# Kernel optimization log

Measured on AMD Instinct MI355X. Metric: run time of the kernel, lower is better.

Reference implementation:

```python
import jax, jax.numpy as jnp
import numpy as np

H = 4
HD = 32
C = 128
NU = 40000
NI = 40000
E = 200000


def _linear(x, W, b):
    # torch Linear: y = x @ W.T + b, W is [out, in]
    return x @ W.T + b


def _counts_in(query, sorted_keys):
    l = jnp.searchsorted(sorted_keys, query, side='left')
    r = jnp.searchsorted(sorted_keys, query, side='right')
    return (r - l).astype(jnp.float32)


def _segment_softmax(scores, seg, n):
    # scores: [E, H], seg: [E] destination ids
    m = jax.ops.segment_max(scores, seg, num_segments=n)
    m = jnp.where(jnp.isfinite(m), m, 0.0)
    e = jnp.exp(scores - m[seg])
    z = jax.ops.segment_sum(e, seg, num_segments=n)
    return e / z[seg]


def _deg_count(idx, n):
    return jnp.zeros((n,), jnp.float32).at[idx].add(1.0)


def _layernorm(x):
    mu = x.mean(-1, keepdims=True)
    var = ((x - mu) ** 2).mean(-1, keepdims=True)
    return (x - mu) / jnp.sqrt(var + 1e-5)


def _relation(x_src, x_dst, src, dst, t_src, t_dst,
              Wq, bq, Wk, bk, Wv, bv, Wo, bo,
              head_bias, beta, tau_raw, gamma, delta,
              counts, recips, n_dst):
    Q = _linear(x_dst, Wq, bq).reshape(-1, H, HD)
    K = _linear(x_src, Wk, bk).reshape(-1, H, HD)
    V = _linear(x_src, Wv, bv).reshape(-1, H, HD)
    Qe, Ke, Ve = Q[dst], K[src], V[src]                      # [E, H, HD]
    scores = (Qe * Ke).sum(-1) / jnp.sqrt(jnp.float32(HD))   # [E, H]
    scores = scores + head_bias
    dt = jnp.abs(t_dst[dst] - t_src[src]) + 1e-6
    tau = jax.nn.softplus(tau_raw) + 1e-6
    scores = scores + (-jnp.log1p(dt / tau))[:, None] * beta
    scores = scores + jnp.log1p(counts)[:, None] * gamma
    scores = scores + recips[:, None] * delta
    w = _segment_softmax(scores, dst, n_dst)                 # [E, H]
    out_e = (Ve * w[:, :, None]).reshape(-1, C)
    out_e = _linear(out_e, Wo, bo)
    return jnp.zeros((n_dst, C), x_dst.dtype).at[dst].add(out_e)


def setup_inputs() -> dict:
    key = jax.random.key(0)
    ks = jax.random.split(key, 20)
    inp = {
        'x_user': jax.random.normal(ks[0], (NU, C), jnp.float32),
        'x_item': jax.random.normal(ks[1], (NI, C), jnp.float32),
        't_user': jax.random.uniform(ks[2], (NU,), jnp.float32) * 100.0,
        't_item': jax.random.uniform(ks[3], (NI,), jnp.float32) * 100.0,
        'edge_index_ui': jax.random.randint(ks[4], (2, E), 0, NU, jnp.int32),
        'edge_index_iu': jax.random.randint(ks[5], (2, E), 0, NI, jnp.int32),
        'Wq': jax.random.normal(ks[6], (C, C), jnp.float32) * 0.05,
        'bq': jax.random.normal(ks[7], (C,), jnp.float32) * 0.05,
        'Wk': jax.random.normal(ks[8], (C, C), jnp.float32) * 0.05,
        'bk': jax.random.normal(ks[9], (C,), jnp.float32) * 0.05,
        'Wv': jax.random.normal(ks[10], (C, C), jnp.float32) * 0.05,
        'bv': jax.random.normal(ks[11], (C,), jnp.float32) * 0.05,
        'Wo': jax.random.normal(ks[12], (C, C), jnp.float32) * 0.05,
        'bo': jax.random.normal(ks[13], (C,), jnp.float32) * 0.05,
        'rel_head_bias': jax.random.normal(ks[14], (2, H), jnp.float32) * 0.1,
        'time_beta': jax.random.normal(ks[15], (2, H), jnp.float32) * 0.1,
        'time_tau_raw': jax.random.normal(ks[16], (2,), jnp.float32),
        'gamma_multirel': jax.random.normal(ks[17], (2, H), jnp.float32) * 0.1,
        'delta_recip': jax.random.normal(ks[18], (2, H), jnp.float32) * 0.1,
    }
    return inp


def reference(x_user, x_item, t_user, t_item, edge_index_ui, edge_index_iu,
              Wq, bq, Wk, bk, Wv, bv, Wo, bo,
              rel_head_bias, time_beta, time_tau_raw, gamma_multirel, delta_recip):
    su, du = edge_index_ui[0], edge_index_ui[1]   # user -> item
    si, di = edge_index_iu[0], edge_index_iu[1]   # item -> user
    # multirel counts (pair multiplicity - 1) and reciprocity flags, per relation
    pid_ui = su * NI + du            # (user,item) pair ids (fits int32: NU*NI < 2^31)
    pid_iu = si * NU + di            # (item,user) pair ids
    rev_for_ui = di * NI + si        # reversed pairs of iu edges in (user,item) space
    rev_for_iu = du * NU + su        # reversed pairs of ui edges in (item,user) space
    counts_ui = _counts_in(pid_ui, jnp.sort(pid_ui)) - 1.0
    counts_iu = _counts_in(pid_iu, jnp.sort(pid_iu)) - 1.0
    recips_ui = (_counts_in(pid_ui, jnp.sort(rev_for_ui)) > 0).astype(jnp.float32)
    recips_iu = (_counts_in(pid_iu, jnp.sort(rev_for_iu)) > 0).astype(jnp.float32)

    out_item = _relation(x_user, x_item, su, du, t_user, t_item,
                         Wq, bq, Wk, bk, Wv, bv, Wo, bo,
                         rel_head_bias[0], time_beta[0], time_tau_raw[0],
                         gamma_multirel[0], delta_recip[0], counts_ui, recips_ui, NI)
    out_user = _relation(x_item, x_user, si, di, t_item, t_user,
                         Wq, bq, Wk, bk, Wv, bv, Wo, bo,
                         rel_head_bias[1], time_beta[1], time_tau_raw[1],
                         gamma_multirel[1], delta_recip[1], counts_iu, recips_iu, NU)
    # degree centrality bias: total (in + out) degree added to every channel
    deg_user = _deg_count(su, NU) + _deg_count(di, NU)
    deg_item = _deg_count(du, NI) + _deg_count(si, NI)
    out_user = out_user + deg_user[:, None]
    out_item = out_item + deg_item[:, None]
    return _layernorm(out_user + x_user), _layernorm(out_item + x_item)
```

## Files before the change

### kernel.cpp

```cpp
#include <hip/hip_runtime.h>
#include <math.h>

constexpr int kH  = 4;
constexpr int kHD = 32;
constexpr int kC  = 128;
constexpr int kNU = 40000;
constexpr int kNI = 40000;
constexpr int kE  = 200000;
constexpr int kNT = kNU + kNI;
constexpr int kSB = (kNT + 1023) / 1024;
constexpr int kTilesPerSide = kNU / 16;
constexpr int kTiles = kNT / 16;
constexpr int kGemmBlocks  = 768;
constexpr int kTableBlocks = 1536;
constexpr int kFusedBlocks = 2304;

#define DEV_INLINE __device__ __forceinline__

typedef short bf16x8 __attribute__((ext_vector_type(8)));
typedef float f32x4  __attribute__((ext_vector_type(4)));
typedef uint32_t u32x4 __attribute__((ext_vector_type(4)));
typedef unsigned long long u64;

DEV_INLINE unsigned short f2bf(float f) {
  uint32_t u = __float_as_uint(f);
  u += 0x7fffu + ((u >> 16) & 1u);
  return (unsigned short)(u >> 16);
}

DEV_INLINE float bflo(uint32_t u) { return __uint_as_float(u << 16); }
DEV_INLINE float bfhi(uint32_t u) { return __uint_as_float(u & 0xffff0000u); }

DEV_INLINE int swz(int row, int elem) {
  return (elem & 7) | (((elem >> 3) ^ (row & 7)) << 3);
}

DEV_INLINE int rpf(const int* __restrict__ rp, const int* __restrict__ boff, int i) {
  return rp[i] + boff[i >> 10];
}

__global__ void cast4w_bf16(const float* __restrict__ w0, const float* __restrict__ w1,
                            const float* __restrict__ w2, const float* __restrict__ w3,
                            unsigned short* __restrict__ o0, unsigned short* __restrict__ o1,
                            unsigned short* __restrict__ o2, unsigned short* __restrict__ o3) {
  int i = blockIdx.x * blockDim.x + threadIdx.x;
  int m = i >> 12, j = i & 4095;
  const float* in = (m == 0) ? w0 : (m == 1) ? w1 : (m == 2) ? w2 : w3;
  unsigned short* out = (m == 0) ? o0 : (m == 1) ? o1 : (m == 2) ? o2 : o3;
  float4 v = ((const float4*)in)[j];
  ushort4 o = {f2bf(v.x), f2bf(v.y), f2bf(v.z), f2bf(v.w)};
  ((ushort4*)out)[j] = o;
}

__global__ __launch_bounds__(256, 3) void qkv_build(
    const float* __restrict__ Xu, const float* __restrict__ Xi,
    const unsigned short* __restrict__ Wq, const unsigned short* __restrict__ Wk,
    const unsigned short* __restrict__ Wv,
    const float* __restrict__ bq, const float* __restrict__ bk,
    const float* __restrict__ bv,
    unsigned short* __restrict__ Qu, unsigned short* __restrict__ Ku,
    unsigned short* __restrict__ Vu,
    unsigned short* __restrict__ Qi, unsigned short* __restrict__ Ki,
    unsigned short* __restrict__ Vi,
    const int* __restrict__ du, const int* __restrict__ di,
    int* __restrict__ deg_all, int* __restrict__ pos_all) {
  __shared__ unsigned short sx[16 * kC];
  __shared__ unsigned short sr[3 * 16 * kC];
  const int bid = blockIdx.x;
  const int tid = threadIdx.x;

  if (bid % 3 != 1) {
    const int tb = (bid / 3) * 2 + ((bid % 3) ? 1 : 0);
    for (int t = tb * 256 + tid; t < 2 * kE; t += kTableBlocks * 256) {
      if (t < kE) {
        pos_all[t] = atomicAdd(&deg_all[du[t]], 1);
      } else {
        pos_all[t] = atomicAdd(&deg_all[kNI + di[t - kE]], 1);
      }
    }
    return;
  }

  const int gb   = bid / 3;
  const int wave = tid >> 6;
  const int lane = tid & 63;
  const int mr   = lane & 15;
  const int quad = lane >> 4;
  const int ct0  = wave * 2;
  const int srow = tid >> 4;
  const int schk = tid & 15;

  bf16x8 wf[3][2][4];
  {
    const unsigned short* Ws[3] = {Wq, Wk, Wv};
#pragma unroll
    for (int m = 0; m < 3; ++m)
#pragma unroll
      for (int c = 0; c < 2; ++c) {
        const unsigned short* wrow = Ws[m] + (size_t)((ct0 + c) * 16 + mr) * kC + quad * 8;
#pragma unroll
        for (int kc = 0; kc < 4; ++kc) wf[m][c][kc] = *(const bf16x8*)(wrow + kc * 32);
      }
  }

  int tile = gb;
  float4 xa, xb;
  {
    const bool item = tile >= kTilesPerSide;
    const float* X = item ? Xi : Xu;
    const int base = (item ? tile - kTilesPerSide : tile) * 16;
    const float* xr = X + (size_t)(base + srow) * kC + schk * 8;
    xa = ((const float4*)xr)[0];
    xb = ((const float4*)xr)[1];
  }

  for (; tile < kTiles; tile += kGemmBlocks) {
    const bool item = tile >= kTilesPerSide;
    const int base = (item ? tile - kTilesPerSide : tile) * 16;

    {
      bf16x8 p;
      p[0] = (short)f2bf(xa.x); p[1] = (short)f2bf(xa.y);
      p[2] = (short)f2bf(xa.z); p[3] = (short)f2bf(xa.w);
      p[4] = (short)f2bf(xb.x); p[5] = (short)f2bf(xb.y);
      p[6] = (short)f2bf(xb.z); p[7] = (short)f2bf(xb.w);
      *(bf16x8*)(sx + srow * kC + ((schk ^ (srow & 7)) << 3)) = p;
    }
    __syncthreads();

    bf16x8 b[4];
#pragma unroll
    for (int kc = 0; kc < 4; ++kc)
      b[kc] = *(const bf16x8*)(sx + mr * kC + (((quad + kc * 4) ^ (mr & 7)) << 3));

    int ntile = tile + kGemmBlocks;
    if (ntile < kTiles) {
      const bool nit = ntile >= kTilesPerSide;
      const float* X = nit ? Xi : Xu;
      const int nbase = (nit ? ntile - kTilesPerSide : ntile) * 16;
      const float* xr = X + (size_t)(nbase + srow) * kC + schk * 8;
      xa = ((const float4*)xr)[0];
      xb = ((const float4*)xr)[1];
    }

    f32x4 acc[3][2];
#pragma unroll
    for (int m = 0; m < 3; ++m) {
      acc[m][0] = (f32x4){0.f, 0.f, 0.f, 0.f};
      acc[m][1] = (f32x4){0.f, 0.f, 0.f, 0.f};
    }
#pragma unroll
    for (int kc = 0; kc < 4; ++kc)
#pragma unroll
      for (int m = 0; m < 3; ++m)
#pragma unroll
        for (int c = 0; c < 2; ++c)
          acc[m][c] = __builtin_amdgcn_mfma_f32_16x16x32_bf16(wf[m][c][kc], b[kc], acc[m][c], 0, 0, 0);

    const float* bs[3] = {bq, bk, bv};
#pragma unroll
    for (int m = 0; m < 3; ++m)
#pragma unroll
      for (int c = 0; c < 2; ++c) {
        int c0 = (ct0 + c) * 16 + quad * 4;
        float4 bb = *(const float4*)(bs[m] + c0);
        uint2 p;
        p.x = (uint32_t)f2bf(acc[m][c][0] + bb.x) | ((uint32_t)f2bf(acc[m][c][1] + bb.y) << 16);
        p.y = (uint32_t)f2bf(acc[m][c][2] + bb.z) | ((uint32_t)f2bf(acc[m][c][3] + bb.w) << 16);
        *(uint2*)(sr + (m * 16 + mr) * kC + swz(mr, c0)) = p;
      }
    __syncthreads();

    {
      unsigned short* Os[3] = {item ? Qi : Qu, item ? Ki : Ku, item ? Vi : Vu};
      const int el = (schk ^ (srow & 7)) << 3;
#pragma unroll
      for (int m = 0; m < 3; ++m) {
        bf16x8 v = *(const bf16x8*)(sr + (m * 16 + srow) * kC + el);
        *(bf16x8*)(Os[m] + (size_t)(base + srow) * kC + schk * 8) = v;
      }
    }
  }
}

__global__ __launch_bounds__(256) void scan1(const int* __restrict__ in,
                                             int* __restrict__ out,
                                             int* __restrict__ bsum, int n) {
  __shared__ int sh[256];
  const int t = threadIdx.x;
  const int base = blockIdx.x * 1024 + t * 4;
  int4 v = {0, 0, 0, 0};
  if (base + 3 < n) {
    v = *(const int4*)(in + base);
  } else {
    if (base + 0 < n) v.x = in[base + 0];
    if (base + 1 < n) v.y = in[base + 1];
    if (base + 2 < n) v.z = in[base + 2];
    if (base + 3 < n) v.w = in[base + 3];
  }
  int s = v.x + v.y + v.z + v.w;
  sh[t] = s;
  __syncthreads();
  int val = s;
  for (int off = 1; off < 256; off <<= 1) {
    int add = (t >= off) ? sh[t - off] : 0;
    __syncthreads();
    val += add;
    sh[t] = val;
    __syncthreads();
  }
  int excl = val - s;
  if (base + 0 < n) out[base + 0] = excl;
  if (base + 1 < n) out[base + 1] = excl + v.x;
  if (base + 2 < n) out[base + 2] = excl + v.x + v.y;
  if (base + 3 < n) out[base + 3] = excl + v.x + v.y + v.z;
  if (t == 255) bsum[blockIdx.x] = val;
}

__global__ __launch_bounds__(128) void scan2(const int* __restrict__ bsum,
                                             int* __restrict__ boff,
                                             int* __restrict__ rp_tail, int nb) {
  __shared__ int sh[128];
  const int t = threadIdx.x;
  int v = (t < nb) ? bsum[t] : 0;
  sh[t] = v;
  __syncthreads();
  int val = v;
  for (int off = 1; off < 128; off <<= 1) {
    int add = (t >= off) ? sh[t - off] : 0;
    __syncthreads();
    val += add;
    sh[t] = val;
    __syncthreads();
  }
  if (t < nb) boff[t] = val - v;
  if (t == nb - 1) *rp_tail = v;
}

__global__ void scatter_pk(const int* __restrict__ su, const int* __restrict__ du,
                           const int* __restrict__ si, const int* __restrict__ di,
                           const int* __restrict__ rp_all, const int* __restrict__ boff,
                           const int* __restrict__ pos_all,
                           u64* __restrict__ el_all) {
  int t = blockIdx.x * blockDim.x + threadIdx.x;
  if (t >= 2 * kE) return;
  int e, s, dg;
  if (t < kE) { e = t;       s = su[e]; dg = du[e]; }
  else        { e = t - kE;  s = si[e]; dg = kNI + di[e]; }
  el_all[rpf(rp_all, boff, dg) + pos_all[t]] = (u64)(uint32_t)e | ((u64)(uint32_t)s << 32);
}

__global__ void bias_csr(const int* __restrict__ su, const int* __restrict__ du,
                         const int* __restrict__ si, const int* __restrict__ di,
                         const float* __restrict__ t_user, const float* __restrict__ t_item,
                         const int* __restrict__ rp_all, const int* __restrict__ boff,
                         const u64* __restrict__ el_all,
                         const float* __restrict__ hb, const float* __restrict__ beta,
                         const float* __restrict__ taur,
                         const float* __restrict__ gamma, const float* __restrict__ delta,
                         float4* __restrict__ bias_ui, float4* __restrict__ bias_iu) {
  int t = blockIdx.x * blockDim.x + threadIdx.x;
  if (t >= 2 * kE) return;
  const int rel = (t >= kE) ? 1 : 0;
  const int e = rel ? t - kE : t;
  int s, d; float ts, td; int dg, rg;
  if (rel == 0) {
    s = su[e]; d = du[e]; ts = t_user[s]; td = t_item[d];
    dg = d;
    rg = kNI + s;
  } else {
    s = si[e]; d = di[e]; ts = t_item[s]; td = t_user[d];
    dg = kNI + d;
    rg = s;
  }
  int b0 = rpf(rp_all, boff, dg), b1 = rpf(rp_all, boff, dg + 1);
  int cnt = 0;
  for (int p = b0; p < b1; ++p) cnt += ((int)(el_all[p] >> 32) == s);
  int r0 = rpf(rp_all, boff, rg), r1 = rpf(rp_all, boff, rg + 1);
  int rcp = 0;
  for (int p = r0; p < r1; ++p) rcp |= ((int)(el_all[p] >> 32) == d);

  float cntv = (float)(cnt - 1);
  float rec  = (float)rcp;
  float dt   = fabsf(td - ts) + 1e-6f;
  float tau  = log1pf(expf(taur[rel])) + 1e-6f;
  float tterm = -log1pf(dt / tau);
  float lc    = log1pf(cntv);
  const float* hp = hb + rel * kH;
  const float* bp = beta + rel * kH;
  const float* gp = gamma + rel * kH;
  const float* dp = delta + rel * kH;
  const float kL2E = 1.4426950408889634f;
  float4 b;
  b.x = (hp[0] + bp[0] * tterm + gp[0] * lc + dp[0] * rec) * kL2E;
  b.y = (hp[1] + bp[1] * tterm + gp[1] * lc + dp[1] * rec) * kL2E;
  b.z = (hp[2] + bp[2] * tterm + gp[2] * lc + dp[2] * rec) * kL2E;
  b.w = (hp[3] + bp[3] * tterm + gp[3] * lc + dp[3] * rec) * kL2E;
  (rel ? bias_iu : bias_ui)[e] = b;
}

__global__ __launch_bounds__(256) void attn_agg(
    const int* __restrict__ rp_all, const int* __restrict__ boff,
    const u64* __restrict__ el_all,
    const unsigned short* __restrict__ Qi, const unsigned short* __restrict__ Ku,
    const unsigned short* __restrict__ Vu,
    const unsigned short* __restrict__ Qu, const unsigned short* __restrict__ Ki,
    const unsigned short* __restrict__ Vi,
    const float* __restrict__ bias_ui, const float* __restrict__ bias_iu,
    unsigned short* __restrict__ h_ui, unsigned short* __restrict__ h_iu) {
  const int wave = threadIdx.x >> 6;
  const int lane = threadIdx.x & 63;
  const int grp  = lane >> 4;
  const int sub  = lane & 15;
  const int h    = sub >> 2;
  const int ch0  = h * kHD + (sub & 3) * 8;
  const int g = blockIdx.x * 4 + wave;
  if (g >= kNT) return;
  const bool isU = g >= kNI;
  const int n = isU ? g - kNI : g;
  const unsigned short* Q = isU ? Qu : Qi;
  const unsigned short* K = isU ? Ki : Ku;
  const unsigned short* V = isU ? Vi : Vu;
  const float* bias = isU ? bias_iu : bias_ui;
  unsigned short* out = isU ? h_iu : h_ui;

  const int beg = rpf(rp_all, boff, g), end = rpf(rp_all, boff, g + 1);
  const float kScaleL2E = 1.4426950408889634f * 0.17677669529663687f;

  float qf[8];
  {
    u32x4 qv = *(const u32x4*)(Q + (size_t)n * kC + ch0);
#pragma unroll
    for (int w = 0; w < 4; ++w) { qf[2 * w] = bflo(qv[w]); qf[2 * w + 1] = bfhi(qv[w]); }
  }

  float z = 0.f;
  float acc[8] = {0.f, 0.f, 0.f, 0.f, 0.f, 0.f, 0.f, 0.f};

  const int p0 = beg + grp;
  int eA = 0, sA = 0;
  if (p0 < end) { u64 pk = el_all[p0]; eA = (int)pk; sA = (int)(pk >> 32); }
  int eB = 0, sB = 0;
  if (p0 + 4 < end) { u64 pk = el_all[p0 + 4]; eB = (int)pk; sB = (int)(pk >> 32); }
  u32x4 kA = *(const u32x4*)(K + (size_t)sA * kC + ch0);
  u32x4 vA = *(const u32x4*)(V + (size_t)sA * kC + ch0);
  float bA = bias[eA * 4 + h];

  for (int p = p0; p < end; p += 4) {
    u32x4 kB = *(const u32x4*)(K + (size_t)sB * kC + ch0);
    u32x4 vB = *(const u32x4*)(V + (size_t)sB * kC + ch0);
    float bB = bias[eB * 4 + h];
    int eC = 0, sC = 0;
    if (p + 8 < end) { u64 pk = el_all[p + 8]; eC = (int)pk; sC = (int)(pk >> 32); }

    float d0 = qf[0] * bflo(kA[0]);
    float d1 = qf[1] * bfhi(kA[0]);
    d0 = fmaf(qf[2], bflo(kA[1]), d0);
    d1 = fmaf(qf[3], bfhi(kA[1]), d1);
    d0 = fmaf(qf[4], bflo(kA[2]), d0);
    d1 = fmaf(qf[5], bfhi(kA[2]), d1);
    d0 = fmaf(qf[6], bflo(kA[3]), d0);
    d1 = fmaf(qf[7], bfhi(kA[3]), d1);
    float dsc = d0 + d1;
    dsc += __shfl_xor(dsc, 1);
    dsc += __shfl_xor(dsc, 2);
    float wgt = __builtin_amdgcn_exp2f(fmaf(dsc, kScaleL2E, bA));
    z += wgt;
#pragma unroll
    for (int w = 0; w < 4; ++w) {
      acc[2 * w]     = fmaf(bflo(vA[w]), wgt, acc[2 * w]);
      acc[2 * w + 1] = fmaf(bfhi(vA[w]), wgt, acc[2 * w + 1]);
    }
    kA = kB; vA = vB; bA = bB; eB = eC; sB = sC;
  }

#pragma unroll
  for (int j = 0; j < 8; ++j) {
    acc[j] += __shfl_xor(acc[j], 16);
    acc[j] += __shfl_xor(acc[j], 32);
  }
  z += __shfl_xor(z, 16);
  z += __shfl_xor(z, 32);

  const float zi = (end > beg) ? 1.0f / z : 0.0f;
  if (grp == 0) {
    bf16x8 o;
#pragma unroll
    for (int j = 0; j < 8; ++j) o[j] = (short)f2bf(acc[j] * zi);
    *(bf16x8*)(out + (size_t)n * kC + ch0) = o;
  }
}

__global__ __launch_bounds__(256, 4) void wo_ln(
    const unsigned short* __restrict__ Hiu, const unsigned short* __restrict__ Hui,
    const unsigned short* __restrict__ Wo,
    const float* __restrict__ Xu, const float* __restrict__ Xi,
    const int* __restrict__ degU, const int* __restrict__ degI,
    const float* __restrict__ bo, float* __restrict__ out) {
  __shared__ unsigned short sh_h[16 * kC];
  __shared__ float sh_p[64 * 2];
  const int tid  = threadIdx.x;
  const int wave = tid >> 6;
  const int lane = tid & 63;
  const int mr   = lane & 15;
  const int quad = lane >> 4;
  const int ct0  = wave * 2;
  const int srow = tid >> 4;
  const int schk = tid & 15;

  bf16x8 wf[2][4];
#pragma unroll
  for (int c = 0; c < 2; ++c) {
    const unsigned short* wrow = Wo + (size_t)((ct0 + c) * 16 + mr) * kC + quad * 8;
#pragma unroll
    for (int kc = 0; kc < 4; ++kc) wf[c][kc] = *(const bf16x8*)(wrow + kc * 32);
  }
  float4 bb[2];
  bb[0] = *(const float4*)(bo + ct0 * 16 + quad * 4);
  bb[1] = *(const float4*)(bo + (ct0 + 1) * 16 + quad * 4);

  int tile = blockIdx.x;
  bf16x8 hv;
  {
    const bool item = tile >= kTilesPerSide;
    const unsigned short* Hs = item ? Hui : Hiu;
    const int base = (item ? tile - kTilesPerSide : tile) * 16;
    hv = *(const bf16x8*)(Hs + (size_t)(base + srow) * kC + schk * 8);
  }

  for (; tile < kTiles; tile += gridDim.x) {
    const bool item = tile >= kTilesPerSide;
    const int base = (item ? tile - kTilesPerSide : tile) * 16;

    *(bf16x8*)(sh_h + srow * kC + ((schk ^ (srow & 7)) << 3)) = hv;
    __syncthreads();

    bf16x8 b[4];
#pragma unroll
    for (int kc = 0; kc < 4; ++kc)
      b[kc] = *(const bf16x8*)(sh_h + mr * kC + (((quad + kc * 4) ^ (mr & 7)) << 3));

    int ntile = tile + gridDim.x;
    if (ntile < kTiles) {
      const bool nit = ntile >= kTilesPerSide;
      const unsigned short* Hs = nit ? Hui : Hiu;
      const int nbase = (nit ? ntile - kTilesPerSide : ntile) * 16;
      hv = *(const bf16x8*)(Hs + (size_t)(nbase + srow) * kC + schk * 8);
    }

    f32x4 acc[2];
    acc[0] = (f32x4){0.f, 0.f, 0.f, 0.f};
    acc[1] = (f32x4){0.f, 0.f, 0.f, 0.f};
#pragma unroll
    for (int kc = 0; kc < 4; ++kc) {
      acc[0] = __builtin_amdgcn_mfma_f32_16x16x32_bf16(wf[0][kc], b[kc], acc[0], 0, 0, 0);
      acc[1] = __builtin_amdgcn_mfma_f32_16x16x32_bf16(wf[1][kc], b[kc], acc[1], 0, 0, 0);
    }

    const int n = base + mr;
    const float* Xs = item ? Xi : Xu;
    const float fdg = (float)(item ? degI[n] : degU[n]);
    float y[8], s1 = 0.f, s2 = 0.f;
#pragma unroll
    for (int c = 0; c < 2; ++c) {
      int c0 = (ct0 + c) * 16 + quad * 4;
      float4 xv = *(const float4*)(Xs + (size_t)n * kC + c0);
      y[c * 4 + 0] = acc[c][0] + xv.x + fdg * bb[c].x;
      y[c * 4 + 1] = acc[c][1] + xv.y + fdg * bb[c].y;
      y[c * 4 + 2] = acc[c][2] + xv.z + fdg * bb[c].z;
      y[c * 4 + 3] = acc[c][3] + xv.w + fdg * bb[c].w;
#pragma unroll
      for (int j = 0; j < 4; ++j) {
        s1 += y[c * 4 + j];
        s2 += y[c * 4 + j] * y[c * 4 + j];
      }
    }
    s1 += __shfl_xor(s1, 16); s2 += __shfl_xor(s2, 16);
    s1 += __shfl_xor(s1, 32); s2 += __shfl_xor(s2, 32);
    if (quad == 0) {
      sh_p[(wave * 16 + mr) * 2]     = s1;
      sh_p[(wave * 16 + mr) * 2 + 1] = s2;
    }
    __syncthreads();
    float t1 = 0.f, t2 = 0.f;
#pragma unroll
    for (int ww = 0; ww < 4; ++ww) {
      t1 += sh_p[(ww * 16 + mr) * 2];
      t2 += sh_p[(ww * 16 + mr) * 2 + 1];
    }
    float mu   = t1 * (1.0f / 128.0f);
    float var  = t2 * (1.0f / 128.0f) - mu * mu;
    float rstd = rsqrtf(fmaxf(var, 0.0f) + 1e-5f);
    float* op = out + (item ? (size_t)kNU * kC : (size_t)0) + (size_t)n * kC;
#pragma unroll
    for (int c = 0; c < 2; ++c) {
      int c0 = (ct0 + c) * 16 + quad * 4;
      float4 o = {(y[c * 4 + 0] - mu) * rstd, (y[c * 4 + 1] - mu) * rstd,
                  (y[c * 4 + 2] - mu) * rstd, (y[c * 4 + 3] - mu) * rstd};
      *(float4*)(op + c0) = o;
    }
  }
}

extern "C" void kernel_launch(void* const* d_in, const int* in_sizes, int n_in,
                              void* d_out, int out_size, void* d_ws, size_t ws_size,
                              hipStream_t stream) {
  const float* x_user = (const float*)d_in[0];
  const float* x_item = (const float*)d_in[1];
  const float* t_user = (const float*)d_in[2];
  const float* t_item = (const float*)d_in[3];
  const int*   eui    = (const int*)d_in[4];
  const int*   eiu    = (const int*)d_in[5];
  const float* Wq = (const float*)d_in[6];
  const float* bq = (const float*)d_in[7];
  const float* Wk = (const float*)d_in[8];
  const float* bk = (const float*)d_in[9];
  const float* Wv = (const float*)d_in[10];
  const float* bv = (const float*)d_in[11];
  const float* Wo = (const float*)d_in[12];
  const float* bo = (const float*)d_in[13];
  const float* hb    = (const float*)d_in[14];
  const float* beta  = (const float*)d_in[15];
  const float* taur  = (const float*)d_in[16];
  const float* gamma = (const float*)d_in[17];
  const float* delta = (const float*)d_in[18];

  const int* su = eui;       const int* du = eui + kE;
  const int* si = eiu;       const int* di = eiu + kE;

  float* w = (float*)d_ws;
  size_t o = 0;
  unsigned short* qu_b = (unsigned short*)(w + o); o += (size_t)kNU * kC / 2;
  unsigned short* ku_b = (unsigned short*)(w + o); o += (size_t)kNU * kC / 2;
  unsigned short* vu_b = (unsigned short*)(w + o); o += (size_t)kNU * kC / 2;
  unsigned short* qi_b = (unsigned short*)(w + o); o += (size_t)kNI * kC / 2;
  unsigned short* ki_b = (unsigned short*)(w + o); o += (size_t)kNI * kC / 2;
  unsigned short* vi_b = (unsigned short*)(w + o); o += (size_t)kNI * kC / 2;
  unsigned short* h_ui = (unsigned short*)(w + o); o += (size_t)kNI * kC / 2;
  unsigned short* h_iu = (unsigned short*)(w + o); o += (size_t)kNU * kC / 2;
  unsigned short* wq_b = (unsigned short*)(w + o); o += kC * kC / 2;
  unsigned short* wk_b = (unsigned short*)(w + o); o += kC * kC / 2;
  unsigned short* wv_b = (unsigned short*)(w + o); o += kC * kC / 2;
  unsigned short* wo_b = (unsigned short*)(w + o); o += kC * kC / 2;
  float* zero_base = w + o;
  int* deg_all = (int*)(w + o); o += kNT;
  size_t zero_bytes = (size_t)((w + o) - zero_base) * sizeof(float);
  float* bias_ui = w + o; o += (size_t)kE * kH;
  float* bias_iu = w + o; o += (size_t)kE * kH;
  int* rp_all  = (int*)(w + o); o += kNT + 1;
  int* bsum    = (int*)(w + o); o += kSB;
  int* boff    = (int*)(w + o); o += kSB;
  o = (o + 1) & ~(size_t)1;
  u64* el_all  = (u64*)(w + o); o += (size_t)2 * kE * 2;
  int* pos_all = (int*)h_ui;

  hipMemsetAsync(zero_base, 0, zero_bytes, stream);

  dim3 b256(256);
  cast4w_bf16<<<(4 * kC * kC / 4) / 256, b256, 0, stream>>>(Wq, Wk, Wv, Wo,
                                                            wq_b, wk_b, wv_b, wo_b);

  qkv_build<<<kFusedBlocks, b256, 0, stream>>>(
      x_user, x_item, wq_b, wk_b, wv_b, bq, bk, bv,
      qu_b, ku_b, vu_b, qi_b, ki_b, vi_b,
      du, di, deg_all, pos_all);

  scan1<<<kSB, b256, 0, stream>>>(deg_all, rp_all, bsum, kNT);
  scan2<<<1, dim3(128), 0, stream>>>(bsum, boff, rp_all + kNT, kSB);

  int g2E = (2 * kE + 255) / 256;
  scatter_pk<<<g2E, b256, 0, stream>>>(su, du, si, di, rp_all, boff, pos_all, el_all);

  bias_csr<<<g2E, b256, 0, stream>>>(su, du, si, di, t_user, t_item,
                                     rp_all, boff, el_all,
                                     hb, beta, taur, gamma, delta,
                                     (float4*)bias_ui, (float4*)bias_iu);

  attn_agg<<<kNT / 4, b256, 0, stream>>>(rp_all, boff, el_all,
                                         qi_b, ku_b, vu_b, qu_b, ki_b, vi_b,
                                         bias_ui, bias_iu, h_ui, h_iu);

  wo_ln<<<768, b256, 0, stream>>>(h_iu, h_ui, wo_b, x_user, x_item,
                                  deg_all + kNI, deg_all, bo, (float*)d_out);
}
```

Measured before the change: 254.5 us.

## Fold weight bf16 casts into GEMM kernels and rebalance block roles

Removes the separate weight-cast kernel. The qkv and output-projection kernels now load fp32 weights and convert them to bf16 in registers, which saves one launch. The fused qkv kernel's block split is flipped so two thirds of the blocks do the GEMM and one third builds the degree/position tables. Launch bounds rise to 6 blocks per CU, the attention edge loop gets unroll 2, and wo_ln launches 1536 blocks. The risks are redundant per-block conversion work and register pressure that could spill under the higher occupancy bound.

```diff
diff --git a/kernel.cpp b/kernel.cpp
--- a/kernel.cpp
+++ b/kernel.cpp
@@ -11,8 +11,8 @@
 constexpr int kSB = (kNT + 1023) / 1024;
 constexpr int kTilesPerSide = kNU / 16;
 constexpr int kTiles = kNT / 16;
-constexpr int kGemmBlocks  = 768;
-constexpr int kTableBlocks = 1536;
+constexpr int kGemmBlocks  = 1536;
+constexpr int kTableBlocks = 768;
 constexpr int kFusedBlocks = 2304;
 
 #define DEV_INLINE __device__ __forceinline__
@@ -39,23 +39,21 @@
   return rp[i] + boff[i >> 10];
 }
 
-__global__ void cast4w_bf16(const float* __restrict__ w0, const float* __restrict__ w1,
-                            const float* __restrict__ w2, const float* __restrict__ w3,
-                            unsigned short* __restrict__ o0, unsigned short* __restrict__ o1,
-                            unsigned short* __restrict__ o2, unsigned short* __restrict__ o3) {
-  int i = blockIdx.x * blockDim.x + threadIdx.x;
-  int m = i >> 12, j = i & 4095;
-  const float* in = (m == 0) ? w0 : (m == 1) ? w1 : (m == 2) ? w2 : w3;
-  unsigned short* out = (m == 0) ? o0 : (m == 1) ? o1 : (m == 2) ? o2 : o3;
-  float4 v = ((const float4*)in)[j];
-  ushort4 o = {f2bf(v.x), f2bf(v.y), f2bf(v.z), f2bf(v.w)};
-  ((ushort4*)out)[j] = o;
-}
-
-__global__ __launch_bounds__(256, 3) void qkv_build(
+DEV_INLINE bf16x8 wload8(const float* __restrict__ wrow) {
+  float4 a = ((const float4*)wrow)[0];
+  float4 b = ((const float4*)wrow)[1];
+  bf16x8 p;
+  p[0] = (short)f2bf(a.x); p[1] = (short)f2bf(a.y);
+  p[2] = (short)f2bf(a.z); p[3] = (short)f2bf(a.w);
+  p[4] = (short)f2bf(b.x); p[5] = (short)f2bf(b.y);
+  p[6] = (short)f2bf(b.z); p[7] = (short)f2bf(b.w);
+  return p;
+}
+
+__global__ __launch_bounds__(256, 6) void qkv_build(
     const float* __restrict__ Xu, const float* __restrict__ Xi,
-    const unsigned short* __restrict__ Wq, const unsigned short* __restrict__ Wk,
-    const unsigned short* __restrict__ Wv,
+    const float* __restrict__ Wq, const float* __restrict__ Wk,
+    const float* __restrict__ Wv,
     const float* __restrict__ bq, const float* __restrict__ bk,
     const float* __restrict__ bv,
     unsigned short* __restrict__ Qu, unsigned short* __restrict__ Ku,
@@ -69,8 +67,8 @@
   const int bid = blockIdx.x;
   const int tid = threadIdx.x;
 
-  if (bid % 3 != 1) {
-    const int tb = (bid / 3) * 2 + ((bid % 3) ? 1 : 0);
+  if (bid % 3 == 1) {
+    const int tb = bid / 3;
     for (int t = tb * 256 + tid; t < 2 * kE; t += kTableBlocks * 256) {
       if (t < kE) {
         pos_all[t] = atomicAdd(&deg_all[du[t]], 1);
@@ -81,7 +79,7 @@
     return;
   }
 
-  const int gb   = bid / 3;
+  const int gb   = (bid / 3) * 2 + (bid % 3 == 2 ? 1 : 0);
   const int wave = tid >> 6;
   const int lane = tid & 63;
   const int mr   = lane & 15;
@@ -92,14 +90,14 @@
 
   bf16x8 wf[3][2][4];
   {
-    const unsigned short* Ws[3] = {Wq, Wk, Wv};
+    const float* Ws[3] = {Wq, Wk, Wv};
 #pragma unroll
     for (int m = 0; m < 3; ++m)
 #pragma unroll
       for (int c = 0; c < 2; ++c) {
-        const unsigned short* wrow = Ws[m] + (size_t)((ct0 + c) * 16 + mr) * kC + quad * 8;
-#pragma unroll
-        for (int kc = 0; kc < 4; ++kc) wf[m][c][kc] = *(const bf16x8*)(wrow + kc * 32);
+        const float* wrow = Ws[m] + (size_t)((ct0 + c) * 16 + mr) * kC + quad * 8;
+#pragma unroll
+        for (int kc = 0; kc < 4; ++kc) wf[m][c][kc] = wload8(wrow + kc * 32);
       }
   }
 
@@ -346,6 +344,7 @@
   u32x4 vA = *(const u32x4*)(V + (size_t)sA * kC + ch0);
   float bA = bias[eA * 4 + h];
 
+#pragma unroll 2
   for (int p = p0; p < end; p += 4) {
     u32x4 kB = *(const u32x4*)(K + (size_t)sB * kC + ch0);
     u32x4 vB = *(const u32x4*)(V + (size_t)sB * kC + ch0);
@@ -391,9 +390,9 @@
   }
 }
 
-__global__ __launch_bounds__(256, 4) void wo_ln(
+__global__ __launch_bounds__(256, 6) void wo_ln(
     const unsigned short* __restrict__ Hiu, const unsigned short* __restrict__ Hui,
-    const unsigned short* __restrict__ Wo,
+    const float* __restrict__ Wo,
     const float* __restrict__ Xu, const float* __restrict__ Xi,
     const int* __restrict__ degU, const int* __restrict__ degI,
     const float* __restrict__ bo, float* __restrict__ out) {
@@ -411,9 +410,9 @@
   bf16x8 wf[2][4];
 #pragma unroll
   for (int c = 0; c < 2; ++c) {
-    const unsigned short* wrow = Wo + (size_t)((ct0 + c) * 16 + mr) * kC + quad * 8;
-#pragma unroll
-    for (int kc = 0; kc < 4; ++kc) wf[c][kc] = *(const bf16x8*)(wrow + kc * 32);
+    const float* wrow = Wo + (size_t)((ct0 + c) * 16 + mr) * kC + quad * 8;
+#pragma unroll
+    for (int kc = 0; kc < 4; ++kc) wf[c][kc] = wload8(wrow + kc * 32);
   }
   float4 bb[2];
   bb[0] = *(const float4*)(bo + ct0 * 16 + quad * 4);
@@ -538,10 +537,6 @@
   unsigned short* vi_b = (unsigned short*)(w + o); o += (size_t)kNI * kC / 2;
   unsigned short* h_ui = (unsigned short*)(w + o); o += (size_t)kNI * kC / 2;
   unsigned short* h_iu = (unsigned short*)(w + o); o += (size_t)kNU * kC / 2;
-  unsigned short* wq_b = (unsigned short*)(w + o); o += kC * kC / 2;
-  unsigned short* wk_b = (unsigned short*)(w + o); o += kC * kC / 2;
-  unsigned short* wv_b = (unsigned short*)(w + o); o += kC * kC / 2;
-  unsigned short* wo_b = (unsigned short*)(w + o); o += kC * kC / 2;
   float* zero_base = w + o;
   int* deg_all = (int*)(w + o); o += kNT;
   size_t zero_bytes = (size_t)((w + o) - zero_base) * sizeof(float);
@@ -557,11 +552,9 @@
   hipMemsetAsync(zero_base, 0, zero_bytes, stream);
 
   dim3 b256(256);
-  cast4w_bf16<<<(4 * kC * kC / 4) / 256, b256, 0, stream>>>(Wq, Wk, Wv, Wo,
-                                                            wq_b, wk_b, wv_b, wo_b);
 
   qkv_build<<<kFusedBlocks, b256, 0, stream>>>(
-      x_user, x_item, wq_b, wk_b, wv_b, bq, bk, bv,
+      x_user, x_item, Wq, Wk, Wv, bq, bk, bv,
       qu_b, ku_b, vu_b, qi_b, ki_b, vi_b,
       du, di, deg_all, pos_all);
 
@@ -580,6 +573,6 @@
                                          qi_b, ku_b, vu_b, qu_b, ki_b, vi_b,
                                          bias_ui, bias_iu, h_ui, h_iu);
 
-  wo_ln<<<768, b256, 0, stream>>>(h_iu, h_ui, wo_b, x_user, x_item,
-                                  deg_all + kNI, deg_all, bo, (float*)d_out);
-}
+  wo_ln<<<kGemmBlocks, b256, 0, stream>>>(h_iu, h_ui, Wo, x_user, x_item,
+                                          deg_all + kNI, deg_all, bo, (float*)d_out);
+}
```

Result: slower. 487.4 us (+91.5%).
